# Kernel tuning notes

Measured on AMD Instinct MI355X. Metric: run time of the kernel, lower is better.

Reference implementation:

```python
import jax, jax.numpy as jnp
import numpy as np

N, E, D, H, G, C = 50000, 800000, 3, 128, 64, 10

def setup_inputs() -> dict:
    key = jax.random.key(0)
    ks = jax.random.split(key, 10)
    s = 0.1  # small init scale
    return {
        "pos": jax.random.normal(ks[0], (N, D), jnp.float32),
        "edge_index": jax.random.randint(ks[1], (2, E), 0, N, dtype=jnp.int64),
        "batch": jnp.sort(jax.random.randint(ks[2], (N,), 0, G, dtype=jnp.int64)),
        "W1": jax.random.normal(ks[3], (D, H), jnp.float32) * s,
        "b1": jnp.zeros((H,), jnp.float32),
        "W2": jax.random.normal(ks[4], (H, H), jnp.float32) * s,
        "b2": jnp.zeros((H,), jnp.float32),
        "W3": jax.random.normal(ks[5], (H, H), jnp.float32) * s,
        "b3": jnp.zeros((H,), jnp.float32),
        "Wl1": jax.random.normal(ks[6], (H, H // 2), jnp.float32) * s,
        "bl1": jnp.zeros((H // 2,), jnp.float32),
        "Wl2": jax.random.normal(ks[7], (H // 2, C), jnp.float32) * s,
        "bl2": jnp.zeros((C,), jnp.float32),
        "num_graphs": G,
    }

def reference(pos, edge_index, batch, W1, b1, W2, b2, W3, b3, Wl1, bl1, Wl2, bl2, num_graphs):
    n = pos.shape[0]
    loop = jnp.arange(n, dtype=edge_index.dtype)
    # GCN: add self-loops, symmetric normalization deg^-1/2 (A+I) deg^-1/2
    src = jnp.concatenate([edge_index[0], loop])
    dst = jnp.concatenate([edge_index[1], loop])
    deg = jax.ops.segment_sum(jnp.ones(src.shape, pos.dtype), dst, num_segments=n)
    dinv = jax.lax.rsqrt(jnp.maximum(deg, 1e-12))  # deg >= 1 due to self-loops
    norm = dinv[src] * dinv[dst]  # [E+N]

    def gcn(x, W, b):
        h = x @ W                               # [N,F] dense transform first (PyG order)
        msg = h[src] * norm[:, None]            # gather + normalize
        return jax.ops.segment_sum(msg, dst, num_segments=n) + b  # scatter-add

    x = jax.nn.relu(gcn(pos, W1, b1))   # dropout = identity (eval mode)
    x = jax.nn.relu(gcn(x, W2, b2))
    x = jax.nn.relu(gcn(x, W3, b3))
    # global_mean_pool over batch ids
    sums = jax.ops.segment_sum(x, batch, num_segments=num_graphs)
    cnt = jax.ops.segment_sum(jnp.ones((n,), x.dtype), batch, num_segments=num_graphs)
    g = sums / jnp.maximum(cnt, 1.0)[:, None]   # [G,H]
    h = jax.nn.relu(g @ Wl1 + bl1)
    return h @ Wl2 + bl2
```

## Files before the change

kernel.cpp:

```cpp
#include <hip/hip_runtime.h>

#define H 128
#define CAP 64
#define LSTRIDE 136
#define PSTR 132
typedef unsigned int uint32;
typedef unsigned short ushort16;
typedef __attribute__((ext_vector_type(8))) short bf16x8;
typedef __attribute__((ext_vector_type(4))) float f32x4;

static __device__ __forceinline__ ushort16 f2bf(float f){
  uint32 u = __float_as_uint(f);
  uint32 r = (u + 0x7fff + ((u >> 16) & 1)) >> 16;
  return (ushort16)r;
}
static __device__ __forceinline__ float bflo(uint32 u){ return __uint_as_float(u << 16); }
static __device__ __forceinline__ float bfhi(uint32 u){ return __uint_as_float(u & 0xffff0000u); }

__global__ __launch_bounds__(256) void k_setup(int* __restrict__ deg, float* __restrict__ gsum,
                                               const int* __restrict__ batch, int n, int G,
                                               int* __restrict__ gb, int SB,
                                               const float* __restrict__ W2, const float* __restrict__ W3,
                                               ushort16* __restrict__ wp2, ushort16* __restrict__ wp3,
                                               float4* __restrict__ y0,
                                               unsigned short* __restrict__ ybA,
                                               unsigned short* __restrict__ ybB){
  int b = blockIdx.x;
  if (b < SB){
    int i = b*256 + threadIdx.x;
    if (i < n) deg[i] = 0;
    if (i < G*H) gsum[i] = 0.f;
    if (i < H){ ybA[(size_t)n*H + i] = 0; ybB[(size_t)n*H + i] = 0; }
    if (i == 0) y0[n] = make_float4(0.f, 0.f, 0.f, 0.f);
    if (i <= G){
      int lo = 0, hi = n;
      while (lo < hi){ int m = (lo + hi) >> 1; if (batch[m] < i) lo = m + 1; else hi = m; }
      gb[i] = lo;
    }
  } else {
    int gid = (b - SB)*256 + threadIdx.x;
    const float* W = (gid < 2048) ? W2 : W3;
    ushort16* wp   = (gid < 2048) ? wp2 : wp3;
    int tid = gid & 2047;
    int frag = tid >> 6, lane = tid & 63;
    int kt = frag >> 3, ct = frag & 7;
    int m = lane & 15, quad = lane >> 4;
    const float* wrow = &W[(kt*32 + quad*8)*H + ct*16 + m];
    ushort16 vals[8];
    #pragma unroll
    for (int j = 0; j < 8; j++) vals[j] = f2bf(wrow[j*H]);
    uint4 o;
    o.x = (uint32)vals[0] | ((uint32)vals[1] << 16);
    o.y = (uint32)vals[2] | ((uint32)vals[3] << 16);
    o.z = (uint32)vals[4] | ((uint32)vals[5] << 16);
    o.w = (uint32)vals[6] | ((uint32)vals[7] << 16);
    *(uint4*)&wp[(size_t)tid*8] = o;
  }
}

__global__ __launch_bounds__(256) void k_fill(const int* __restrict__ src, const int* __restrict__ dst,
                                              int E, int* __restrict__ deg,
                                              unsigned short* __restrict__ csr_src){
  int base = (blockIdx.x*256 + threadIdx.x) * 4;
  if (base + 3 < E){
    int4 d = *(const int4*)&dst[base];
    int4 s = *(const int4*)&src[base];
    int t0 = atomicAdd(&deg[d.x], 1);
    int t1 = atomicAdd(&deg[d.y], 1);
    int t2 = atomicAdd(&deg[d.z], 1);
    int t3 = atomicAdd(&deg[d.w], 1);
    if (t0 < CAP) csr_src[((size_t)d.x << 6) + t0] = (unsigned short)s.x;
    if (t1 < CAP) csr_src[((size_t)d.y << 6) + t1] = (unsigned short)s.y;
    if (t2 < CAP) csr_src[((size_t)d.z << 6) + t2] = (unsigned short)s.z;
    if (t3 < CAP) csr_src[((size_t)d.w << 6) + t3] = (unsigned short)s.w;
  } else if (base < E){
    for (int i = base; i < E; i++){
      int d = dst[i];
      int t = atomicAdd(&deg[d], 1);
      if (t < CAP) csr_src[((size_t)d << 6) + t] = (unsigned short)src[i];
    }
  }
}

__global__ __launch_bounds__(256) void k_pre(const int* __restrict__ deg, const float* __restrict__ pos,
                                             float4* __restrict__ y0, int n){
  int i = blockIdx.x*256 + threadIdx.x;
  if (i < n){
    float dv = rsqrtf((float)(deg[i] + 1));
    y0[i] = make_float4(pos[3*i]*dv, pos[3*i+1]*dv, pos[3*i+2]*dv, 0.f);
  }
}

__global__ __launch_bounds__(256) void k_layer1(const float4* __restrict__ y0, const int* __restrict__ deg,
      const unsigned short* __restrict__ csr_src,
      const float* __restrict__ W1, const float* __restrict__ b1,
      ushort16* __restrict__ y1, int n){
  int node = blockIdx.x*256 + threadIdx.x;
  if (node >= n) return;
  int cnt = deg[node];
  int lo = node << 6;
  float4 own = y0[node];
  float x = own.x, y = own.y, z = own.z;
  int mm = cnt > CAP ? CAP : cnt;
  int nfull = mm >> 3, rem = mm & 7;
  #define GADD(s0,s1,s2,s3,s4,s5,s6,s7) { \
    float4 v0 = y0[s0], v1 = y0[s1], v2 = y0[s2], v3 = y0[s3]; \
    float4 v4 = y0[s4], v5 = y0[s5], v6 = y0[s6], v7 = y0[s7]; \
    x += ((v0.x+v1.x)+(v2.x+v3.x)) + ((v4.x+v5.x)+(v6.x+v7.x)); \
    y += ((v0.y+v1.y)+(v2.y+v3.y)) + ((v4.y+v5.y)+(v6.y+v7.y)); \
    z += ((v0.z+v1.z)+(v2.z+v3.z)) + ((v4.z+v5.z)+(v6.z+v7.z)); }
  if (rem){
    uint4 iv = *(const uint4*)&csr_src[lo + nfull*8];
    int s0 = (int)(iv.x & 0xffff);
    int s1 = (1 < rem)? (int)(iv.x >> 16)    : n;
    int s2 = (2 < rem)? (int)(iv.y & 0xffff) : n;
    int s3 = (3 < rem)? (int)(iv.y >> 16)    : n;
    int s4 = (4 < rem)? (int)(iv.z & 0xffff) : n;
    int s5 = (5 < rem)? (int)(iv.z >> 16)    : n;
    int s6 = (6 < rem)? (int)(iv.w & 0xffff) : n;
    int s7 = (7 < rem)? (int)(iv.w >> 16)    : n;
    GADD(s0,s1,s2,s3,s4,s5,s6,s7);
  }
  if (nfull){
    uint4 iv = *(const uint4*)&csr_src[lo];
    for (int c = 0; c < nfull; c++){
      uint4 nx = *(const uint4*)&csr_src[lo + c*8 + 8];
      int s0 = iv.x & 0xffff, s1 = iv.x >> 16;
      int s2 = iv.y & 0xffff, s3 = iv.y >> 16;
      int s4 = iv.z & 0xffff, s5 = iv.z >> 16;
      int s6 = iv.w & 0xffff, s7 = iv.w >> 16;
      GADD(s0,s1,s2,s3,s4,s5,s6,s7);
      iv = nx;
    }
  }
  #undef GADD
  float dn = rsqrtf((float)(cnt + 1));
  x *= dn; y *= dn; z *= dn;
  ushort16* rowp = &y1[(size_t)node*H];
  for (int c8 = 0; c8 < 16; c8++){
    float4 wa0 = *(const float4*)&W1[c8*8];
    float4 wa1 = *(const float4*)&W1[c8*8+4];
    float4 wb0 = *(const float4*)&W1[H + c8*8];
    float4 wb1 = *(const float4*)&W1[H + c8*8+4];
    float4 wc0 = *(const float4*)&W1[2*H + c8*8];
    float4 wc1 = *(const float4*)&W1[2*H + c8*8+4];
    float4 bb0 = *(const float4*)&b1[c8*8];
    float4 bb1 = *(const float4*)&b1[c8*8+4];
    float o0 = fmaxf(x*wa0.x + y*wb0.x + z*wc0.x + bb0.x, 0.f) * dn;
    float o1 = fmaxf(x*wa0.y + y*wb0.y + z*wc0.y + bb0.y, 0.f) * dn;
    float o2 = fmaxf(x*wa0.z + y*wb0.z + z*wc0.z + bb0.z, 0.f) * dn;
    float o3 = fmaxf(x*wa0.w + y*wb0.w + z*wc0.w + bb0.w, 0.f) * dn;
    float o4 = fmaxf(x*wa1.x + y*wb1.x + z*wc1.x + bb1.x, 0.f) * dn;
    float o5 = fmaxf(x*wa1.y + y*wb1.y + z*wc1.y + bb1.y, 0.f) * dn;
    float o6 = fmaxf(x*wa1.z + y*wb1.z + z*wc1.z + bb1.z, 0.f) * dn;
    float o7 = fmaxf(x*wa1.w + y*wb1.w + z*wc1.w + bb1.w, 0.f) * dn;
    uint4 o;
    o.x = (uint32)f2bf(o0) | ((uint32)f2bf(o1) << 16);
    o.y = (uint32)f2bf(o2) | ((uint32)f2bf(o3) << 16);
    o.z = (uint32)f2bf(o4) | ((uint32)f2bf(o5) << 16);
    o.w = (uint32)f2bf(o6) | ((uint32)f2bf(o7) << 16);
    *(uint4*)&rowp[c8*8] = o;
  }
}

template<int POOL>
__global__ __launch_bounds__(256) void k_aggdense(const ushort16* __restrict__ y, const int* __restrict__ deg,
      const unsigned short* __restrict__ csr_src, const ushort16* __restrict__ wp,
      const float* __restrict__ bias,
      ushort16* __restrict__ yout, const int* __restrict__ batch, float* __restrict__ gsum, int n){
  __shared__ unsigned short As[16*LSTRIDE];
  __shared__ float pool[POOL ? 16*PSTR : 1];
  __shared__ unsigned short outs[POOL ? 1 : 16*PSTR];
  __shared__ int sbatch[POOL ? 16 : 1];
  __shared__ float sdinv[POOL ? 1 : 16];
  int tid = threadIdx.x;
  int node16 = blockIdx.x*16;
  int nl = tid >> 4;
  int node = node16 + nl;
  int f8 = (tid & 15) * 8;

  if (tid < 16){
    int nn = node16 + tid;
    if (POOL) sbatch[tid] = (nn < n) ? batch[nn] : -1;
    else      sdinv[tid]  = (nn < n) ? rsqrtf((float)(deg[nn] + 1)) : 0.f;
  }

  float a0=0,a1=0,a2=0,a3=0,a4=0,a5=0,a6=0,a7=0;
  float dn = 0.f;
  #define ADDU(u) { a0+=bflo(u.x); a1+=bfhi(u.x); a2+=bflo(u.y); a3+=bfhi(u.y); \
                    a4+=bflo(u.z); a5+=bfhi(u.z); a6+=bflo(u.w); a7+=bfhi(u.w); }
  #define GATHER8(s0,s1,s2,s3,s4,s5,s6,s7) { \
    uint4 u0 = *(const uint4*)&y[(size_t)(s0)*H + f8]; \
    uint4 u1 = *(const uint4*)&y[(size_t)(s1)*H + f8]; \
    uint4 u2 = *(const uint4*)&y[(size_t)(s2)*H + f8]; \
    uint4 u3 = *(const uint4*)&y[(size_t)(s3)*H + f8]; \
    uint4 u4 = *(const uint4*)&y[(size_t)(s4)*H + f8]; \
    uint4 u5 = *(const uint4*)&y[(size_t)(s5)*H + f8]; \
    uint4 u6 = *(const uint4*)&y[(size_t)(s6)*H + f8]; \
    uint4 u7 = *(const uint4*)&y[(size_t)(s7)*H + f8]; \
    ADDU(u0); ADDU(u1); ADDU(u2); ADDU(u3); \
    ADDU(u4); ADDU(u5); ADDU(u6); ADDU(u7); }
  if (node < n){
    int cnt = deg[node];
    int lo = node << 6;
    dn = rsqrtf((float)(cnt + 1));
    uint4 uo = *(const uint4*)&y[(size_t)node*H + f8];
    ADDU(uo);
    int mm = cnt > CAP ? CAP : cnt;
    int nfull = mm >> 3, rem = mm & 7;
    if (rem){
      uint4 iv = *(const uint4*)&csr_src[lo + nfull*8];
      int s0 = (int)(iv.x & 0xffff);
      int s1 = (1 < rem)? (int)(iv.x >> 16)    : n;
      int s2 = (2 < rem)? (int)(iv.y & 0xffff) : n;
      int s3 = (3 < rem)? (int)(iv.y >> 16)    : n;
      int s4 = (4 < rem)? (int)(iv.z & 0xffff) : n;
      int s5 = (5 < rem)? (int)(iv.z >> 16)    : n;
      int s6 = (6 < rem)? (int)(iv.w & 0xffff) : n;
      int s7 = (7 < rem)? (int)(iv.w >> 16)    : n;
      GATHER8(s0,s1,s2,s3,s4,s5,s6,s7);
    }
    if (nfull){
      uint4 iv = *(const uint4*)&csr_src[lo];
      for (int c = 0; c < nfull; c++){
        uint4 nx = *(const uint4*)&csr_src[lo + c*8 + 8];
        int s0 = iv.x & 0xffff, s1 = iv.x >> 16;
        int s2 = iv.y & 0xffff, s3 = iv.y >> 16;
        int s4 = iv.z & 0xffff, s5 = iv.z >> 16;
        int s6 = iv.w & 0xffff, s7 = iv.w >> 16;
        GATHER8(s0,s1,s2,s3,s4,s5,s6,s7);
        iv = nx;
      }
    }
  }
  #undef GATHER8
  #undef ADDU
  uint4 o;
  o.x = (uint32)f2bf(a0*dn) | ((uint32)f2bf(a1*dn) << 16);
  o.y = (uint32)f2bf(a2*dn) | ((uint32)f2bf(a3*dn) << 16);
  o.z = (uint32)f2bf(a4*dn) | ((uint32)f2bf(a5*dn) << 16);
  o.w = (uint32)f2bf(a6*dn) | ((uint32)f2bf(a7*dn) << 16);
  *(uint4*)&As[nl*LSTRIDE + f8] = o;
  __syncthreads();

  int wave = tid >> 6;
  int lane = tid & 63;
  int m = lane & 15, quad = lane >> 4;
  f32x4 acc0 = {0.f,0.f,0.f,0.f}, acc1 = {0.f,0.f,0.f,0.f};
  int ct0 = wave*2, ct1 = wave*2 + 1;
  #pragma unroll
  for (int kt = 0; kt < 4; kt++){
    bf16x8 af = *(const bf16x8*)&As[m*LSTRIDE + kt*32 + quad*8];
    bf16x8 b0 = *(const bf16x8*)&wp[(size_t)((kt*8+ct0)*64 + lane)*8];
    bf16x8 b1 = *(const bf16x8*)&wp[(size_t)((kt*8+ct1)*64 + lane)*8];
    acc0 = __builtin_amdgcn_mfma_f32_16x16x32_bf16(af, b0, acc0, 0, 0, 0);
    acc1 = __builtin_amdgcn_mfma_f32_16x16x32_bf16(af, b1, acc1, 0, 0, 0);
  }
  #pragma unroll
  for (int j = 0; j < 2; j++){
    int ct = wave*2 + j;
    int col = ct*16 + m;
    float bv = bias[col];
    f32x4 ac = j ? acc1 : acc0;
    #pragma unroll
    for (int r = 0; r < 4; r++){
      int rl = quad*4 + r;
      int orow = node16 + rl;
      if (orow < n){
        float v = fmaxf(ac[r] + bv, 0.f);
        if (POOL) pool[rl*PSTR + col] = v;
        else      outs[rl*PSTR + col] = f2bf(v * sdinv[rl]);
      }
    }
  }
  __syncthreads();
  if (POOL){
    int col = tid & 127;
    int half = tid >> 7;
    float run = 0.f; int gprev = -1;
    for (int r = half*8; r < half*8 + 8; r++){
      int g = sbatch[r];
      if (g < 0) break;
      if (g != gprev){
        if (gprev >= 0) atomicAdd(&gsum[gprev*H + col], run);
        run = 0.f; gprev = g;
      }
      run += pool[r*PSTR + col];
    }
    if (gprev >= 0) atomicAdd(&gsum[gprev*H + col], run);
  } else {
    int row = tid >> 4;
    int orow = node16 + row;
    if (orow < n){
      const unsigned short* sp = &outs[row*PSTR + f8];
      uint4 v;
      v.x = (uint32)sp[0] | ((uint32)sp[1] << 16);
      v.y = (uint32)sp[2] | ((uint32)sp[3] << 16);
      v.z = (uint32)sp[4] | ((uint32)sp[5] << 16);
      v.w = (uint32)sp[6] | ((uint32)sp[7] << 16);
      *(uint4*)&yout[(size_t)orow*H + f8] = v;
    }
  }
}

__global__ __launch_bounds__(64) void k_head(const float* __restrict__ gsum, const int* __restrict__ gb,
            const float* __restrict__ Wl1, const float* __restrict__ bl1,
            const float* __restrict__ Wl2, const float* __restrict__ bl2,
            float* __restrict__ out){
  int g = blockIdx.x;
  int t = threadIdx.x;
  __shared__ float gs[H];
  __shared__ float h1[64];
  float inv = 1.f / fmaxf((float)(gb[g+1] - gb[g]), 1.f);
  gs[t]      = gsum[g*H + t]      * inv;
  gs[64 + t] = gsum[g*H + 64 + t] * inv;
  __syncthreads();
  float acc = bl1[t];
  for (int k = 0; k < H; k++) acc += gs[k] * Wl1[k*64 + t];
  h1[t] = fmaxf(acc, 0.f);
  __syncthreads();
  if (t < 10){
    float o = bl2[t];
    for (int j = 0; j < 64; j++) o += h1[j] * Wl2[j*10 + t];
    out[g*10 + t] = o;
  }
}

extern "C" void kernel_launch(void* const* d_in, const int* in_sizes, int n_in,
                              void* d_out, int out_size, void* d_ws, size_t ws_size,
                              hipStream_t stream){
  const float* pos = (const float*)d_in[0];
  const int*  ei   = (const int*)d_in[1];
  const int*  batch= (const int*)d_in[2];
  const float* W1 = (const float*)d_in[3];
  const float* b1 = (const float*)d_in[4];
  const float* W2 = (const float*)d_in[5];
  const float* b2 = (const float*)d_in[6];
  const float* W3 = (const float*)d_in[7];
  const float* b3 = (const float*)d_in[8];
  const float* Wl1 = (const float*)d_in[9];
  const float* bl1 = (const float*)d_in[10];
  const float* Wl2 = (const float*)d_in[11];
  const float* bl2 = (const float*)d_in[12];
  float* out = (float*)d_out;

  int N = in_sizes[0] / 3;
  int E = in_sizes[1] / 2;
  int G = out_size / 10;
  int SB = (N + 255) / 256;

  char* p = (char*)d_ws;
  auto carve = [&](size_t bytes)->char* { char* q = p; p += (bytes + 255) & ~(size_t)255; return q; };
  int*            deg     = (int*)     carve(sizeof(int)    * (size_t)N);
  int*            gb      = (int*)     carve(sizeof(int)    * (size_t)(G+1));
  float*          gsum    = (float*)   carve(sizeof(float)  * (size_t)G * H);
  unsigned short* csr_src = (unsigned short*)carve(sizeof(unsigned short) * (size_t)(N+1) * CAP);
  float4*         y0      = (float4*)  carve(sizeof(float4) * (size_t)(N+1));
  ushort16*       ybufA   = (ushort16*)carve(sizeof(ushort16) * (size_t)(N+1) * H);
  ushort16*       ybufB   = (ushort16*)carve(sizeof(ushort16) * (size_t)(N+1) * H);
  ushort16*       wp2     = (ushort16*)carve(sizeof(ushort16) * 16384);
  ushort16*       wp3     = (ushort16*)carve(sizeof(ushort16) * 16384);

  const int* src = ei;
  const int* dst = ei + E;

  hipLaunchKernelGGL(k_setup, dim3(SB + 16), dim3(256), 0, stream,
                     deg, gsum, batch, N, G, gb, SB, W2, W3, wp2, wp3,
                     y0, (unsigned short*)ybufA, (unsigned short*)ybufB);

  hipLaunchKernelGGL(k_fill, dim3(((E+3)/4 + 255)/256), dim3(256), 0, stream, src, dst, E, deg, csr_src);

  hipLaunchKernelGGL(k_pre, dim3((N+255)/256), dim3(256), 0, stream, deg, pos, y0, N);

  hipLaunchKernelGGL(k_layer1, dim3((N+255)/256), dim3(256), 0, stream, y0, deg, csr_src, W1, b1, ybufA, N);

  hipLaunchKernelGGL(k_aggdense<0>, dim3((N+15)/16), dim3(256), 0, stream,
                     ybufA, deg, csr_src, wp2, b2, ybufB, (const int*)nullptr, (float*)nullptr, N);

  hipLaunchKernelGGL(k_aggdense<1>, dim3((N+15)/16), dim3(256), 0, stream,
                     ybufB, deg, csr_src, wp3, b3, (ushort16*)nullptr, batch, gsum, N);

  hipLaunchKernelGGL(k_head, dim3(G), dim3(64), 0, stream, gsum, gb, Wl1, bl1, Wl2, bl2, out);
}
```

Before: 226.5 us.

## Split CSR fill into atomic count and separate scatter pass fused with prescale

Replaces the combined atomic-count-and-write kernel with two passes. The first records each edge's atomic rank. The second scatters source ids into the fixed-capacity CSR and also computes the degree-normalized positions, which removes the separate k_pre launch. The aim is to take the dependent scatter store out of the atomic latency path and to drop one launch. In exchange it writes and rereads a rank array and reads dst twice.

```diff
diff --git a/kernel.cpp b/kernel.cpp
--- a/kernel.cpp
+++ b/kernel.cpp
@@ -58,36 +58,30 @@
   }
 }
 
-__global__ __launch_bounds__(256) void k_fill(const int* __restrict__ src, const int* __restrict__ dst,
-                                              int E, int* __restrict__ deg,
-                                              unsigned short* __restrict__ csr_src){
-  int base = (blockIdx.x*256 + threadIdx.x) * 4;
-  if (base + 3 < E){
-    int4 d = *(const int4*)&dst[base];
-    int4 s = *(const int4*)&src[base];
-    int t0 = atomicAdd(&deg[d.x], 1);
-    int t1 = atomicAdd(&deg[d.y], 1);
-    int t2 = atomicAdd(&deg[d.z], 1);
-    int t3 = atomicAdd(&deg[d.w], 1);
-    if (t0 < CAP) csr_src[((size_t)d.x << 6) + t0] = (unsigned short)s.x;
-    if (t1 < CAP) csr_src[((size_t)d.y << 6) + t1] = (unsigned short)s.y;
-    if (t2 < CAP) csr_src[((size_t)d.z << 6) + t2] = (unsigned short)s.z;
-    if (t3 < CAP) csr_src[((size_t)d.w << 6) + t3] = (unsigned short)s.w;
-  } else if (base < E){
-    for (int i = base; i < E; i++){
-      int d = dst[i];
-      int t = atomicAdd(&deg[d], 1);
-      if (t < CAP) csr_src[((size_t)d << 6) + t] = (unsigned short)src[i];
-    }
-  }
-}
-
-__global__ __launch_bounds__(256) void k_pre(const int* __restrict__ deg, const float* __restrict__ pos,
-                                             float4* __restrict__ y0, int n){
+__global__ __launch_bounds__(256) void k_count(const int* __restrict__ dst, int E,
+                                               int* __restrict__ deg, unsigned short* __restrict__ rank){
   int i = blockIdx.x*256 + threadIdx.x;
-  if (i < n){
-    float dv = rsqrtf((float)(deg[i] + 1));
-    y0[i] = make_float4(pos[3*i]*dv, pos[3*i+1]*dv, pos[3*i+2]*dv, 0.f);
+  if (i < E) rank[i] = (unsigned short)atomicAdd(&deg[dst[i]], 1);
+}
+
+__global__ __launch_bounds__(256) void k_scatter(const int* __restrict__ src, const int* __restrict__ dst,
+                                                 int E, int SCB, const unsigned short* __restrict__ rank,
+                                                 unsigned short* __restrict__ csr_src,
+                                                 const int* __restrict__ deg, const float* __restrict__ pos,
+                                                 float4* __restrict__ y0, int n){
+  int b = blockIdx.x;
+  if (b < SCB){
+    int i = b*256 + threadIdx.x;
+    if (i < E){
+      int r = rank[i];
+      if (r < CAP) csr_src[((size_t)dst[i] << 6) + r] = (unsigned short)src[i];
+    }
+  } else {
+    int i = (b - SCB)*256 + threadIdx.x;
+    if (i < n){
+      float dv = rsqrtf((float)(deg[i] + 1));
+      y0[i] = make_float4(pos[3*i]*dv, pos[3*i+1]*dv, pos[3*i+2]*dv, 0.f);
+    }
   }
 }
 
@@ -348,6 +342,8 @@
   int E = in_sizes[1] / 2;
   int G = out_size / 10;
   int SB = (N + 255) / 256;
+  int SCB = (E + 255) / 256;
+  int PB = (N + 255) / 256;
 
   char* p = (char*)d_ws;
   auto carve = [&](size_t bytes)->char* { char* q = p; p += (bytes + 255) & ~(size_t)255; return q; };
@@ -355,6 +351,7 @@
   int*            gb      = (int*)     carve(sizeof(int)    * (size_t)(G+1));
   float*          gsum    = (float*)   carve(sizeof(float)  * (size_t)G * H);
   unsigned short* csr_src = (unsigned short*)carve(sizeof(unsigned short) * (size_t)(N+1) * CAP);
+  unsigned short* rank    = (unsigned short*)carve(sizeof(unsigned short) * (size_t)E);
   float4*         y0      = (float4*)  carve(sizeof(float4) * (size_t)(N+1));
   ushort16*       ybufA   = (ushort16*)carve(sizeof(ushort16) * (size_t)(N+1) * H);
   ushort16*       ybufB   = (ushort16*)carve(sizeof(ushort16) * (size_t)(N+1) * H);
@@ -368,9 +365,10 @@
                      deg, gsum, batch, N, G, gb, SB, W2, W3, wp2, wp3,
                      y0, (unsigned short*)ybufA, (unsigned short*)ybufB);
 
-  hipLaunchKernelGGL(k_fill, dim3(((E+3)/4 + 255)/256), dim3(256), 0, stream, src, dst, E, deg, csr_src);
-
-  hipLaunchKernelGGL(k_pre, dim3((N+255)/256), dim3(256), 0, stream, deg, pos, y0, N);
+  hipLaunchKernelGGL(k_count, dim3((E+255)/256), dim3(256), 0, stream, dst, E, deg, rank);
+
+  hipLaunchKernelGGL(k_scatter, dim3(SCB + PB), dim3(256), 0, stream,
+                     src, dst, E, SCB, rank, csr_src, deg, pos, y0, N);
 
   hipLaunchKernelGGL(k_layer1, dim3((N+255)/256), dim3(256), 0, stream, y0, deg, csr_src, W1, b1, ybufA, N);
 
```

New measurement: 230.8 us. No clear change (+1.9%).
